# Optimization experiments

Measured on AMD Instinct MI355X. Metric: run time of the kernel, lower is better.

The kernel has to match this reference:

```python
import jax, jax.numpy as jnp
import numpy as np

NBLOCK = 2000
DIM = 2048
B, T = 32, 1024
EPS = 1e-12  # F.normalize eps


def _l2norm(v, axis):
    n = jnp.sqrt(jnp.sum(v * v, axis=axis, keepdims=True))
    return v / jnp.maximum(n, EPS)


def setup_inputs() -> dict:
    key = jax.random.key(0)
    kx, km, kw = jax.random.split(key, 3)
    x = jax.random.normal(kx, (B, T, DIM), dtype=jnp.float32)
    mask = jax.random.randint(km, (B, T), 0, 2).astype(jnp.int32)
    stdv = 1.0 / np.sqrt(DIM)
    weight = jax.random.uniform(kw, (NBLOCK, DIM), dtype=jnp.float32,
                                minval=-stdv, maxval=stdv)
    return {"x": x, "mask": mask, "weight": weight}


def reference(x, mask, weight):
    half = x.shape[0] // 2
    nblock = weight.shape[0]
    m = mask.astype(x.dtype)  # [B, T]

    # diversity: || W W^T - I ||_F
    gram = weight @ weight.T  # [N, N]
    diversity_loss = jnp.linalg.norm(gram - jnp.eye(nblock, dtype=weight.dtype))

    # cosine-similarity attention: [B, T, N]
    att = jnp.einsum('btd,nd->btn', _l2norm(x, axis=2), _l2norm(weight, axis=1))

    # uniformity loss: masked sum over T, softmax over blocks, mean over half-batch
    s = jnp.einsum('btn,bt->nb', att[:half], m[:half])  # [N, half]
    tmp = jnp.mean(jax.nn.softmax(s, axis=0), axis=1)   # [N]
    u_loss = jnp.linalg.norm(tmp)

    # per-row min over masked positions of the top-1 similarity
    top1 = jnp.max(att, axis=2)  # [B, T] (only topk[...,0] is used)
    inf = jnp.asarray(jnp.inf, dtype=x.dtype)
    masked_top1 = jnp.where(m > 0, top1, inf)
    min_sim = jnp.min(masked_top1[:half], axis=1)   # [half]
    ab_min = jnp.min(masked_top1[half:], axis=1)    # [half]

    return (0.2 * diversity_loss,
            2.0 - jnp.mean(min_sim) + jnp.mean(ab_min),
            0.5 * u_loss)
```

## Files before the change

kernel.cpp:

```cpp
#include <hip/hip_runtime.h>

typedef unsigned short u16;
typedef unsigned int u32;
typedef __attribute__((ext_vector_type(8))) short short8;
typedef __attribute__((ext_vector_type(8))) u16 ushort8;
typedef __attribute__((ext_vector_type(4))) u16 ushort4_t;
typedef __attribute__((ext_vector_type(4))) float fx4;

#define DIMK 2048
#define NBLK 2000

typedef const __attribute__((address_space(1))) void* gp_t;
typedef __attribute__((address_space(3))) void* lp_t;

__device__ __forceinline__ u16 f2bf(float f) {
  u32 u = __float_as_uint(f);
  u32 r = (u + 0x7fffu + ((u >> 16) & 1u)) >> 16;
  return (u16)r;
}

__device__ __forceinline__ u32 fkey(float f) {
  u32 u = __float_as_uint(f);
  return (u & 0x80000000u) ? ~u : (u | 0x80000000u);
}
__device__ __forceinline__ float dekey(u32 k) {
  u32 u = (k & 0x80000000u) ? (k ^ 0x80000000u) : ~k;
  return __uint_as_float(u);
}

__device__ __forceinline__ void gemm_tile(const u16* __restrict__ Abase,
                                          const u16* __restrict__ Bbase,
                                          int row0, int col0,
                                          u16* lsA, u16* lsB,
                                          fx4 acc[4][4])
{
  const int tid  = threadIdx.x;
  const int wv   = tid >> 6;
  const int lane = tid & 63;
  const int wr   = wv & 1, wc = wv >> 1;
  const int quad = lane >> 4, lc = lane & 15;

  const int srow = wv * 32 + (lane >> 2);
  const int skel = (((lane & 3) ^ ((lane >> 3) & 3)) * 8);
  const u16* gA0 = Abase + (size_t)(row0 + srow) * DIMK + skel;
  const u16* gA1 = gA0 + (size_t)16 * DIMK;
  const u16* gB0 = Bbase + (size_t)(col0 + srow) * DIMK + skel;
  const u16* gB1 = gB0 + (size_t)16 * DIMK;
  u16* lA0 = lsA + wv * 1024;
  u16* lA1 = lsA + wv * 1024 + 512;
  u16* lB0 = lsB + wv * 1024;
  u16* lB1 = lsB + wv * 1024 + 512;

  const int fIntra = lc * 32 + ((quad ^ ((lc >> 1) & 3)) * 8);

#pragma unroll
  for (int mi = 0; mi < 4; mi++)
#pragma unroll
    for (int ni = 0; ni < 4; ni++)
      acc[mi][ni] = fx4{0.f, 0.f, 0.f, 0.f};

  for (int k0 = 0; k0 < DIMK; k0 += 32) {
    __syncthreads();
    __builtin_amdgcn_global_load_lds((gp_t)gA0, (lp_t)lA0, 16, 0, 0);
    __builtin_amdgcn_global_load_lds((gp_t)gA1, (lp_t)lA1, 16, 0, 0);
    __builtin_amdgcn_global_load_lds((gp_t)gB0, (lp_t)lB0, 16, 0, 0);
    __builtin_amdgcn_global_load_lds((gp_t)gB1, (lp_t)lB1, 16, 0, 0);
    gA0 += 32; gA1 += 32; gB0 += 32; gB1 += 32;
    __syncthreads();
    short8 af[4], bfr[4];
#pragma unroll
    for (int mi = 0; mi < 4; mi++)
      af[mi] = *(const short8*)(lsA + (wr * 4 + mi) * 512 + fIntra);
#pragma unroll
    for (int ni = 0; ni < 4; ni++)
      bfr[ni] = *(const short8*)(lsB + (wc * 4 + ni) * 512 + fIntra);
#pragma unroll
    for (int mi = 0; mi < 4; mi++)
#pragma unroll
      for (int ni = 0; ni < 4; ni++)
        acc[mi][ni] = __builtin_amdgcn_mfma_f32_16x16x32_bf16(af[mi], bfr[ni], acc[mi][ni], 0, 0, 0);
  }
}

__global__ __launch_bounds__(256) void norm_rows_x(const float* __restrict__ x,
                                                   u16* __restrict__ Xn)
{
  const int wv = threadIdx.x >> 6, lane = threadIdx.x & 63;
  const int row = blockIdx.x * 4 + wv;
  const float4* xr = (const float4*)(x + (size_t)row * DIMK);
  float4 v[8];
  float ss = 0.f;
#pragma unroll
  for (int j = 0; j < 8; j++) {
    v[j] = xr[j * 64 + lane];
    ss += v[j].x*v[j].x + v[j].y*v[j].y + v[j].z*v[j].z + v[j].w*v[j].w;
  }
#pragma unroll
  for (int off = 1; off < 64; off <<= 1) ss += __shfl_xor(ss, off);
  float inv = 1.0f / fmaxf(sqrtf(ss), 1e-12f);
  ushort4_t* o = (ushort4_t*)(Xn + (size_t)row * DIMK);
#pragma unroll
  for (int j = 0; j < 8; j++) {
    ushort4_t t;
    t[0] = f2bf(v[j].x * inv); t[1] = f2bf(v[j].y * inv);
    t[2] = f2bf(v[j].z * inv); t[3] = f2bf(v[j].w * inv);
    o[j * 64 + lane] = t;
  }
}

__global__ __launch_bounds__(256) void norm_rows_w(const float* __restrict__ w,
                                                   u16* __restrict__ Wn,
                                                   u16* __restrict__ Wb)
{
  const int wv = threadIdx.x >> 6, lane = threadIdx.x & 63;
  const int row = blockIdx.x * 4 + wv;
  ushort4_t* on_ = (ushort4_t*)(Wn + (size_t)row * DIMK);
  ushort4_t* ob_ = (ushort4_t*)(Wb + (size_t)row * DIMK);
  if (row < NBLK) {
    const float4* wr_ = (const float4*)(w + (size_t)row * DIMK);
    float4 v[8];
    float ss = 0.f;
#pragma unroll
    for (int j = 0; j < 8; j++) {
      v[j] = wr_[j * 64 + lane];
      ss += v[j].x*v[j].x + v[j].y*v[j].y + v[j].z*v[j].z + v[j].w*v[j].w;
    }
#pragma unroll
    for (int off = 1; off < 64; off <<= 1) ss += __shfl_xor(ss, off);
    float inv = 1.0f / fmaxf(sqrtf(ss), 1e-12f);
#pragma unroll
    for (int j = 0; j < 8; j++) {
      ushort4_t tn, tb;
      tn[0] = f2bf(v[j].x * inv); tn[1] = f2bf(v[j].y * inv);
      tn[2] = f2bf(v[j].z * inv); tn[3] = f2bf(v[j].w * inv);
      tb[0] = f2bf(v[j].x); tb[1] = f2bf(v[j].y);
      tb[2] = f2bf(v[j].z); tb[3] = f2bf(v[j].w);
      on_[j * 64 + lane] = tn;
      ob_[j * 64 + lane] = tb;
    }
  } else {
    ushort4_t z = ushort4_t{0, 0, 0, 0};
#pragma unroll
    for (int j = 0; j < 8; j++) { on_[j * 64 + lane] = z; ob_[j * 64 + lane] = z; }
  }
}

__global__ __launch_bounds__(256) void gram_kernel(const u16* __restrict__ Wb,
                                                   float* __restrict__ divsum)
{
  __shared__ __align__(16) u16 lsA[4096];
  __shared__ __align__(16) u16 lsB[4096];
  fx4 acc[4][4];
  const int i0 = blockIdx.y * 128, j0 = blockIdx.x * 128;
  gemm_tile(Wb, Wb, i0, j0, lsA, lsB, acc);
  const int tid = threadIdx.x, wv = tid >> 6, lane = tid & 63;
  const int wr = wv & 1, wc = wv >> 1, quad = lane >> 4, lc = lane & 15;
  float local = 0.f;
#pragma unroll
  for (int mi = 0; mi < 4; mi++) {
#pragma unroll
    for (int ni = 0; ni < 4; ni++) {
#pragma unroll
      for (int r = 0; r < 4; r++) {
        int i = i0 + wr * 64 + mi * 16 + quad * 4 + r;
        int j = j0 + wc * 64 + ni * 16 + lc;
        float g = acc[mi][ni][r];
        float d = (i == j && i < NBLK) ? 1.0f : 0.0f;
        float e = g - d;
        local += e * e;
      }
    }
  }
#pragma unroll
  for (int off = 1; off < 64; off <<= 1) local += __shfl_xor(local, off);
  if (lane == 0) atomicAdd(divsum, local);
}

__global__ __launch_bounds__(512, 2) void att_kernel(const u16* __restrict__ Xn,
                                                     const u16* __restrict__ Wn,
                                                     const int* __restrict__ mask,
                                                     u32* __restrict__ top1k,
                                                     float* __restrict__ s)
{
  __shared__ __align__(16) u16 ring[4][2][8192];

  const int orig = blockIdx.x;
  const int wg   = ((orig & 7) << 7) | (orig >> 3);
  const int xb   = wg & 7;
  const int yb   = wg >> 3;
  const int row0 = yb << 8, col0 = xb << 8;

  const int tid  = threadIdx.x;
  const int wv   = tid >> 6, lane = tid & 63;
  const int wr   = wv >> 2, wc = wv & 3;
  const int quad = lane >> 4, lc = lane & 15;

  const int srow = wv * 32 + (lane >> 2);
  const int skel = (((lane & 3) ^ ((lane >> 3) & 3)) << 3);
  const u16* gA0 = Xn + (size_t)(row0 + srow) * DIMK + skel;
  const u16* gA1 = gA0 + (size_t)16 * DIMK;
  const u16* gB0 = Wn + (size_t)(col0 + srow) * DIMK + skel;
  const u16* gB1 = gB0 + (size_t)16 * DIMK;

  const int fIntra = lc * 32 + ((quad ^ ((lc >> 1) & 3)) << 3);

  fx4 acc[8][4];
#pragma unroll
  for (int mi = 0; mi < 8; mi++)
#pragma unroll
    for (int ni = 0; ni < 4; ni++)
      acc[mi][ni] = fx4{0.f, 0.f, 0.f, 0.f};

#define STAGE(slot, kt)                                                          \
  do {                                                                           \
    const int ko_ = (kt) << 5;                                                   \
    u16* lA_ = &ring[(slot)][0][wv << 10];                                       \
    u16* lB_ = &ring[(slot)][1][wv << 10];                                       \
    __builtin_amdgcn_global_load_lds((gp_t)(gA0 + ko_), (lp_t)lA_,         16, 0, 0); \
    __builtin_amdgcn_global_load_lds((gp_t)(gA1 + ko_), (lp_t)(lA_ + 512), 16, 0, 0); \
    __builtin_amdgcn_global_load_lds((gp_t)(gB0 + ko_), (lp_t)lB_,         16, 0, 0); \
    __builtin_amdgcn_global_load_lds((gp_t)(gB1 + ko_), (lp_t)(lB_ + 512), 16, 0, 0); \
  } while (0)

  STAGE(0, 0);
  STAGE(1, 1);
  STAGE(2, 2);

  const int NT = DIMK / 32;
  for (int t = 0; t < NT; ++t) {
    if (t <= NT - 3)      asm volatile("s_waitcnt vmcnt(8)" ::: "memory");
    else if (t == NT - 2) asm volatile("s_waitcnt vmcnt(4)" ::: "memory");
    else                  asm volatile("s_waitcnt vmcnt(0)" ::: "memory");
    __builtin_amdgcn_s_barrier();
    __builtin_amdgcn_sched_barrier(0);

    if (t + 3 < NT) STAGE((t + 3) & 3, t + 3);

    const u16* lAt = &ring[t & 3][0][0];
    const u16* lBt = &ring[t & 3][1][0];
    short8 af[8], bfr[4];
#pragma unroll
    for (int mi = 0; mi < 8; mi++)
      af[mi] = *(const short8*)(lAt + (wr * 8 + mi) * 512 + fIntra);
#pragma unroll
    for (int ni = 0; ni < 4; ni++)
      bfr[ni] = *(const short8*)(lBt + (wc * 4 + ni) * 512 + fIntra);

    __builtin_amdgcn_s_setprio(1);
#pragma unroll
    for (int mi = 0; mi < 8; mi++)
#pragma unroll
      for (int ni = 0; ni < 4; ni++)
        acc[mi][ni] = __builtin_amdgcn_mfma_f32_16x16x32_bf16(af[mi], bfr[ni], acc[mi][ni], 0, 0, 0);
    __builtin_amdgcn_s_setprio(0);
  }
#undef STAGE

#pragma unroll
  for (int mi = 0; mi < 8; mi++) {
#pragma unroll
    for (int r = 0; r < 4; r++) {
      float v = -3.0e38f;
#pragma unroll
      for (int ni = 0; ni < 4; ni++) {
        int col = col0 + wc * 64 + ni * 16 + lc;
        float av = acc[mi][ni][r];
        v = (col < NBLK && av > v) ? av : v;
      }
      v = fmaxf(v, __shfl_xor(v, 1));
      v = fmaxf(v, __shfl_xor(v, 2));
      v = fmaxf(v, __shfl_xor(v, 4));
      v = fmaxf(v, __shfl_xor(v, 8));
      if (lc == 0) {
        int row = row0 + wr * 128 + mi * 16 + quad * 4 + r;
        atomicMax(&top1k[row], fkey(v));
      }
    }
  }

  if (yb < 64) {
    const int b = yb >> 2;
    float sv[4] = {0.f, 0.f, 0.f, 0.f};
#pragma unroll
    for (int mi = 0; mi < 8; mi++) {
#pragma unroll
      for (int r = 0; r < 4; r++) {
        float mval = (float)mask[row0 + wr * 128 + mi * 16 + quad * 4 + r];
#pragma unroll
        for (int ni = 0; ni < 4; ni++)
          sv[ni] += mval * acc[mi][ni][r];
      }
    }
#pragma unroll
    for (int ni = 0; ni < 4; ni++) {
      float v = sv[ni];
      v += __shfl_xor(v, 16);
      v += __shfl_xor(v, 32);
      int col = col0 + wc * 64 + ni * 16 + lc;
      if (quad == 0 && col < NBLK)
        atomicAdd(&s[b * 2048 + col], v);
    }
  }
}

__global__ __launch_bounds__(256) void softmax_kernel(const float* __restrict__ s,
                                                      float* __restrict__ tmp)
{
  const int b = blockIdx.x, tid = threadIdx.x;
  const float* sb = s + b * 2048;
  __shared__ float red[4];
  float mx = -3.0e38f;
  for (int n = tid; n < NBLK; n += 256) mx = fmaxf(mx, sb[n]);
#pragma unroll
  for (int off = 1; off < 64; off <<= 1) mx = fmaxf(mx, __shfl_xor(mx, off));
  if ((tid & 63) == 0) red[tid >> 6] = mx;
  __syncthreads();
  mx = fmaxf(fmaxf(red[0], red[1]), fmaxf(red[2], red[3]));
  __syncthreads();
  float se = 0.f;
  for (int n = tid; n < NBLK; n += 256) se += expf(sb[n] - mx);
#pragma unroll
  for (int off = 1; off < 64; off <<= 1) se += __shfl_xor(se, off);
  if ((tid & 63) == 0) red[tid >> 6] = se;
  __syncthreads();
  se = red[0] + red[1] + red[2] + red[3];
  float scale = 1.0f / (se * 16.0f);
  for (int n = tid; n < NBLK; n += 256) atomicAdd(&tmp[n], expf(sb[n] - mx) * scale);
}

__global__ __launch_bounds__(1024) void finalize_kernel(const u32* __restrict__ top1k,
                                                        const int* __restrict__ mask,
                                                        const float* __restrict__ tmp,
                                                        const float* __restrict__ divsum,
                                                        float* __restrict__ out)
{
  const int tid = threadIdx.x;
  __shared__ float sMin[32];
  __shared__ float sSq[16];
  const int b = tid >> 5, li = tid & 31;
  float mn = 3.0e38f;
  for (int t = li; t < 1024; t += 32) {
    int idx = b * 1024 + t;
    if (mask[idx] > 0) mn = fminf(mn, dekey(top1k[idx]));
  }
#pragma unroll
  for (int off = 1; off < 32; off <<= 1) mn = fminf(mn, __shfl_xor(mn, off));
  if (li == 0) sMin[b] = mn;
  float ssq = 0.f;
  for (int n = tid; n < NBLK; n += 1024) { float v = tmp[n]; ssq += v * v; }
#pragma unroll
  for (int off = 1; off < 64; off <<= 1) ssq += __shfl_xor(ssq, off);
  if ((tid & 63) == 0) sSq[tid >> 6] = ssq;
  __syncthreads();
  if (tid == 0) {
    float m0 = 0.f, m1 = 0.f;
    for (int i = 0; i < 16; i++) { m0 += sMin[i]; m1 += sMin[16 + i]; }
    m0 *= (1.0f / 16.0f); m1 *= (1.0f / 16.0f);
    float sq = 0.f;
    for (int i = 0; i < 16; i++) sq += sSq[i];
    out[0] = 0.2f * sqrtf(divsum[0]);
    out[1] = 2.0f - m0 + m1;
    out[2] = 0.5f * sqrtf(sq);
  }
}

extern "C" void kernel_launch(void* const* d_in, const int* in_sizes, int n_in,
                              void* d_out, int out_size, void* d_ws, size_t ws_size,
                              hipStream_t stream) {
  const float* x    = (const float*)d_in[0];
  const int*   mask = (const int*)d_in[1];
  const float* w    = (const float*)d_in[2];
  float* out = (float*)d_out;

  char* ws = (char*)d_ws;
  u32*   top1k  = (u32*)(ws);
  float* s      = (float*)(ws + 131072);
  float* tmp    = (float*)(ws + 262144);
  float* divsum = (float*)(ws + 270336);
  u16*   Xn     = (u16*)(ws + 270592);
  u16*   Wn     = (u16*)(ws + 270592 + 134217728ull);
  u16*   Wb     = (u16*)(ws + 270592 + 134217728ull + 8388608ull);

  hipMemsetAsync(ws, 0, 270592, stream);

  norm_rows_w<<<dim3(512), dim3(256), 0, stream>>>(w, Wn, Wb);
  norm_rows_x<<<dim3(8192), dim3(256), 0, stream>>>(x, Xn);
  gram_kernel<<<dim3(16, 16), dim3(256), 0, stream>>>(Wb, divsum);
  att_kernel<<<dim3(1024), dim3(512), 0, stream>>>(Xn, Wn, mask, top1k, s);
  softmax_kernel<<<dim3(16), dim3(256), 0, stream>>>(s, tmp);
  finalize_kernel<<<dim3(1), dim3(1024), 0, stream>>>(top1k, mask, tmp, divsum, out);
}
```

Before: 730.3 us.

## Split att k-loop into two MFMA phases with interleaved staging; use gram symmetry

After: 724.7 us. No clear change (-0.8%).

```diff
diff --git a/kernel.cpp b/kernel.cpp
--- a/kernel.cpp
+++ b/kernel.cpp
@@ -148,13 +148,16 @@
 __global__ __launch_bounds__(256) void gram_kernel(const u16* __restrict__ Wb,
                                                    float* __restrict__ divsum)
 {
+  const int bx = blockIdx.x, by = blockIdx.y;
+  if (by > bx) return;
   __shared__ __align__(16) u16 lsA[4096];
   __shared__ __align__(16) u16 lsB[4096];
   fx4 acc[4][4];
-  const int i0 = blockIdx.y * 128, j0 = blockIdx.x * 128;
+  const int i0 = by * 128, j0 = bx * 128;
   gemm_tile(Wb, Wb, i0, j0, lsA, lsB, acc);
   const int tid = threadIdx.x, wv = tid >> 6, lane = tid & 63;
   const int wr = wv & 1, wc = wv >> 1, quad = lane >> 4, lc = lane & 15;
+  const float mult = (bx == by) ? 1.0f : 2.0f;
   float local = 0.f;
 #pragma unroll
   for (int mi = 0; mi < 4; mi++) {
@@ -171,6 +174,7 @@
       }
     }
   }
+  local *= mult;
 #pragma unroll
   for (int off = 1; off < 64; off <<= 1) local += __shfl_xor(local, off);
   if (lane == 0) atomicAdd(divsum, local);
@@ -211,50 +215,70 @@
     for (int ni = 0; ni < 4; ni++)
       acc[mi][ni] = fx4{0.f, 0.f, 0.f, 0.f};
 
-#define STAGE(slot, kt)                                                          \
+#define STAGE_A(kt)                                                              \
   do {                                                                           \
     const int ko_ = (kt) << 5;                                                   \
-    u16* lA_ = &ring[(slot)][0][wv << 10];                                       \
-    u16* lB_ = &ring[(slot)][1][wv << 10];                                       \
+    u16* lA_ = &ring[(kt) & 3][0][wv << 10];                                     \
     __builtin_amdgcn_global_load_lds((gp_t)(gA0 + ko_), (lp_t)lA_,         16, 0, 0); \
     __builtin_amdgcn_global_load_lds((gp_t)(gA1 + ko_), (lp_t)(lA_ + 512), 16, 0, 0); \
+  } while (0)
+#define STAGE_B(kt)                                                              \
+  do {                                                                           \
+    const int ko_ = (kt) << 5;                                                   \
+    u16* lB_ = &ring[(kt) & 3][1][wv << 10];                                     \
     __builtin_amdgcn_global_load_lds((gp_t)(gB0 + ko_), (lp_t)lB_,         16, 0, 0); \
     __builtin_amdgcn_global_load_lds((gp_t)(gB1 + ko_), (lp_t)(lB_ + 512), 16, 0, 0); \
   } while (0)
 
-  STAGE(0, 0);
-  STAGE(1, 1);
-  STAGE(2, 2);
+#define K_ITER(T, VM, DO_STAGE)                                                  \
+  do {                                                                           \
+    const u16* lAt_ = &ring[(T) & 3][0][0];                                      \
+    const u16* lBt_ = &ring[(T) & 3][1][0];                                      \
+    short8 bfr[4], af0[4], af1[4];                                               \
+    _Pragma("unroll") for (int q = 0; q < 4; q++)                                \
+      bfr[q] = *(const short8*)(lBt_ + (wc * 4 + q) * 512 + fIntra);             \
+    _Pragma("unroll") for (int q = 0; q < 4; q++)                                \
+      af0[q] = *(const short8*)(lAt_ + (wr * 8 + q) * 512 + fIntra);             \
+    if (DO_STAGE) STAGE_A((T) + 3);                                              \
+    __builtin_amdgcn_s_barrier();                                                \
+    asm volatile("s_waitcnt lgkmcnt(0)" ::: "memory");                           \
+    __builtin_amdgcn_s_setprio(1);                                               \
+    _Pragma("unroll") for (int mi = 0; mi < 4; mi++)                             \
+      _Pragma("unroll") for (int ni = 0; ni < 4; ni++)                           \
+        acc[mi][ni] = __builtin_amdgcn_mfma_f32_16x16x32_bf16(af0[mi], bfr[ni], acc[mi][ni], 0, 0, 0); \
+    __builtin_amdgcn_s_setprio(0);                                               \
+    __builtin_amdgcn_s_barrier();                                                \
+    _Pragma("unroll") for (int q = 0; q < 4; q++)                                \
+      af1[q] = *(const short8*)(lAt_ + (wr * 8 + 4 + q) * 512 + fIntra);         \
+    if (DO_STAGE) STAGE_B((T) + 3);                                              \
+    asm volatile("s_waitcnt " VM ::: "memory");                                  \
+    __builtin_amdgcn_s_barrier();                                                \
+    asm volatile("s_waitcnt lgkmcnt(0)" ::: "memory");                           \
+    __builtin_amdgcn_s_setprio(1);                                               \
+    _Pragma("unroll") for (int mi = 0; mi < 4; mi++)                             \
+      _Pragma("unroll") for (int ni = 0; ni < 4; ni++)                           \
+        acc[4 + mi][ni] = __builtin_amdgcn_mfma_f32_16x16x32_bf16(af1[mi], bfr[ni], acc[4 + mi][ni], 0, 0, 0); \
+    __builtin_amdgcn_s_setprio(0);                                               \
+    __builtin_amdgcn_s_barrier();                                                \
+  } while (0)
+
+  STAGE_A(0); STAGE_B(0);
+  STAGE_A(1); STAGE_B(1);
+  STAGE_A(2); STAGE_B(2);
+  asm volatile("s_waitcnt vmcnt(8)" ::: "memory");
+  __builtin_amdgcn_s_barrier();
 
   const int NT = DIMK / 32;
-  for (int t = 0; t < NT; ++t) {
-    if (t <= NT - 3)      asm volatile("s_waitcnt vmcnt(8)" ::: "memory");
-    else if (t == NT - 2) asm volatile("s_waitcnt vmcnt(4)" ::: "memory");
-    else                  asm volatile("s_waitcnt vmcnt(0)" ::: "memory");
-    __builtin_amdgcn_s_barrier();
-    __builtin_amdgcn_sched_barrier(0);
-
-    if (t + 3 < NT) STAGE((t + 3) & 3, t + 3);
-
-    const u16* lAt = &ring[t & 3][0][0];
-    const u16* lBt = &ring[t & 3][1][0];
-    short8 af[8], bfr[4];
-#pragma unroll
-    for (int mi = 0; mi < 8; mi++)
-      af[mi] = *(const short8*)(lAt + (wr * 8 + mi) * 512 + fIntra);
-#pragma unroll
-    for (int ni = 0; ni < 4; ni++)
-      bfr[ni] = *(const short8*)(lBt + (wc * 4 + ni) * 512 + fIntra);
-
-    __builtin_amdgcn_s_setprio(1);
-#pragma unroll
-    for (int mi = 0; mi < 8; mi++)
-#pragma unroll
-      for (int ni = 0; ni < 4; ni++)
-        acc[mi][ni] = __builtin_amdgcn_mfma_f32_16x16x32_bf16(af[mi], bfr[ni], acc[mi][ni], 0, 0, 0);
-    __builtin_amdgcn_s_setprio(0);
-  }
-#undef STAGE
+#pragma unroll 1
+  for (int t = 0; t < NT - 4; ++t)
+    K_ITER(t, "vmcnt(8)", 1);
+  K_ITER(NT - 4, "vmcnt(8)", 1);
+  K_ITER(NT - 3, "vmcnt(4)", 0);
+  K_ITER(NT - 2, "vmcnt(0)", 0);
+  K_ITER(NT - 1, "vmcnt(0)", 0);
+#undef K_ITER
+#undef STAGE_A
+#undef STAGE_B
 
 #pragma unroll
   for (int mi = 0; mi < 8; mi++) {
```
